# Optimization experiments

Measured on AMD Instinct MI355X. Metric: run time of the kernel, lower is better.

The kernel has to match this reference:

```python
import jax, jax.numpy as jnp
import numpy as np

TOPK = 8  # n_activated_experts


def setup_inputs() -> dict:
    key = jax.random.key(0)
    k1, k2 = jax.random.split(key)
    tokens, dim, n_experts = 8192, 4096, 64
    x = jax.random.normal(k1, (tokens, dim), dtype=jnp.float32)
    weight = jax.random.normal(k2, (n_experts, dim), dtype=jnp.float32) * 0.02
    bias = jnp.zeros((n_experts,), dtype=jnp.float32)
    return {"x": x, "weight": weight, "bias": bias}


def reference(x, weight, bias):
    # scores: [tokens, n_experts]
    scores = jnp.einsum("td,ed->te", x, weight) + bias
    probs = jax.nn.softmax(scores, axis=-1)  # score_func == 'softmax'
    weights, indices = jax.lax.top_k(probs, TOPK)
    return probs, indices
```

## Files before the change

### kernel.cpp

```cpp
#include <hip/hip_runtime.h>
#include <math.h>

#define NTOK    8192
#define DIM     4096
#define NEXP    64
#define TOPK_N  8
#define TAU     2.0e-4f
#define KSPLIT  8
#define KSTEPS  ((DIM / KSPLIT) / 32)
#define TB      16

#define WS_WHI_OFF  0
#define WS_WLO_OFF  524288

typedef __attribute__((ext_vector_type(8))) short short8;
typedef __attribute__((ext_vector_type(4))) float f32x4;

__device__ __forceinline__ void cvt8(float4 a0, float4 a1, short8& hv, short8& lv) {
    float f[8] = {a0.x, a0.y, a0.z, a0.w, a1.x, a1.y, a1.z, a1.w};
    union { short8 v; unsigned u[4]; } H, L;
    #pragma unroll
    for (int i = 0; i < 4; ++i) {
        unsigned b0 = __float_as_uint(f[2*i]);
        unsigned b1 = __float_as_uint(f[2*i+1]);
        float r0 = f[2*i]   - __uint_as_float(b0 & 0xffff0000u);
        float r1 = f[2*i+1] - __uint_as_float(b1 & 0xffff0000u);
        H.u[i] = (b0 >> 16) | (b1 & 0xffff0000u);
        L.u[i] = (__float_as_uint(r0) >> 16) | (__float_as_uint(r1) & 0xffff0000u);
    }
    hv = H.v; lv = L.v;
}

__global__ __launch_bounds__(256, 4)
void cvt_w_kernel(const float* __restrict__ w, unsigned short* __restrict__ whi,
                  unsigned short* __restrict__ wlo) {
    const int g = blockIdx.x * 256 + threadIdx.x;
    const float* p = w + (size_t)g * 8;
    union { short8 v; uint4 q; } H, L;
    float4 a0 = *(const float4*)(p);
    float4 a1 = *(const float4*)(p + 4);
    cvt8(a0, a1, H.v, L.v);
    *(uint4*)(whi + (size_t)g * 8) = H.q;
    *(uint4*)(wlo + (size_t)g * 8) = L.q;
}

__global__ __launch_bounds__(512, 4)
void gemm_kernel(const float* __restrict__ x, const unsigned short* __restrict__ whi,
                 const unsigned short* __restrict__ wlo, const float* __restrict__ bias,
                 const float* __restrict__ wfp, float* __restrict__ out, int ntok) {
    __shared__ float  lds_part[KSPLIT][TB][65];
    __shared__ float  lds_s[TB][68];
    __shared__ float  top9[TB][9];
    __shared__ double dsc[NEXP];
    __shared__ int    nflag;
    __shared__ int    ftok[TB];
    __shared__ float  fninth[TB];

    const int tid  = threadIdx.x;
    const int lane = tid & 63;
    const int wv   = tid >> 6;
    const int nl   = lane & 15;
    const int q    = lane >> 4;
    const int tok0 = blockIdx.x * TB;
    if (tid == 0) nflag = 0;

    const int kbase = wv * (DIM / KSPLIT);
    const float* xr = x + (size_t)(tok0 + nl) * DIM;
    size_t boff[4];
    #pragma unroll
    for (int nf = 0; nf < 4; ++nf) boff[nf] = (size_t)(nf * 16 + nl) * DIM;

    f32x4 acc[4];
    #pragma unroll
    for (int nf = 0; nf < 4; ++nf) acc[nf] = (f32x4){0.f, 0.f, 0.f, 0.f};

    float4 Ar[2][2];
    short8 Bh[2][4], Bl[2][4];

    {
        const int k0 = kbase + q * 8;
        Ar[0][0] = *(const float4*)(xr + k0);
        Ar[0][1] = *(const float4*)(xr + k0 + 4);
        #pragma unroll
        for (int nf = 0; nf < 4; ++nf) {
            Bh[0][nf] = *(const short8*)(whi + boff[nf] + k0);
            Bl[0][nf] = *(const short8*)(wlo + boff[nf] + k0);
        }
    }

    #pragma unroll 2
    for (int ks = 0; ks < KSTEPS; ++ks) {
        const int buf = ks & 1, nxt = buf ^ 1;
        if (ks + 1 < KSTEPS) {
            const int k1 = kbase + (ks + 1) * 32 + q * 8;
            Ar[nxt][0] = *(const float4*)(xr + k1);
            Ar[nxt][1] = *(const float4*)(xr + k1 + 4);
            #pragma unroll
            for (int nf = 0; nf < 4; ++nf) {
                Bh[nxt][nf] = *(const short8*)(whi + boff[nf] + k1);
                Bl[nxt][nf] = *(const short8*)(wlo + boff[nf] + k1);
            }
        }
        short8 ahi, alo;
        cvt8(Ar[buf][0], Ar[buf][1], ahi, alo);
        #pragma unroll
        for (int nf = 0; nf < 4; ++nf) {
            acc[nf] = __builtin_amdgcn_mfma_f32_16x16x32_bf16(ahi, Bl[buf][nf], acc[nf], 0, 0, 0);
            acc[nf] = __builtin_amdgcn_mfma_f32_16x16x32_bf16(alo, Bh[buf][nf], acc[nf], 0, 0, 0);
            acc[nf] = __builtin_amdgcn_mfma_f32_16x16x32_bf16(ahi, Bh[buf][nf], acc[nf], 0, 0, 0);
        }
    }

    #pragma unroll
    for (int nf = 0; nf < 4; ++nf)
        #pragma unroll
        for (int r = 0; r < 4; ++r)
            lds_part[wv][q * 4 + r][nf * 16 + nl] = acc[nf][r];
    __syncthreads();

    #pragma unroll
    for (int i = 0; i < (TB * NEXP) / 512; ++i) {
        const int p  = tid + i * 512;
        const int tk = p >> 6, e = p & 63;
        float s = lds_part[0][tk][e];
        #pragma unroll
        for (int k = 1; k < KSPLIT; ++k) s += lds_part[k][tk][e];
        lds_s[tk][e] = s + bias[e];
    }
    __syncthreads();

    float* __restrict__ out_idx = out + (size_t)ntok * NEXP;
    #pragma unroll
    for (int t = 0; t < 2; ++t) {
        const int tokl = wv * 2 + t;
        const int tok  = tok0 + tokl;
        const float s  = lds_s[tokl][lane];

        float m = s;
        #pragma unroll
        for (int off = 32; off > 0; off >>= 1)
            m = fmaxf(m, __shfl_xor(m, off, 64));
        const float ex = expf(s - m);
        float sum = ex;
        #pragma unroll
        for (int off = 32; off > 0; off >>= 1)
            sum += __shfl_xor(sum, off, 64);
        out[(size_t)tok * NEXP + lane] = ex / sum;

        int rank = 0;
        #pragma unroll
        for (int i = 0; i < 16; ++i) {
            const float4 v4 = *(const float4*)(&lds_s[tokl][i * 4]);
            rank += (int)((v4.x > s) || (v4.x == s && (i * 4 + 0) < lane));
            rank += (int)((v4.y > s) || (v4.y == s && (i * 4 + 1) < lane));
            rank += (int)((v4.z > s) || (v4.z == s && (i * 4 + 2) < lane));
            rank += (int)((v4.w > s) || (v4.w == s && (i * 4 + 3) < lane));
        }
        if (rank < TOPK_N + 1) top9[tokl][rank] = s;
        if (rank < TOPK_N)
            out_idx[(size_t)tok * TOPK_N + rank] = (float)lane;
    }
    __syncthreads();

    if (tid < TB) {
        float ming = 1e30f;
        #pragma unroll
        for (int r = 0; r < TOPK_N; ++r)
            ming = fminf(ming, top9[tid][r] - top9[tid][r + 1]);
        if (ming < TAU) {
            const int sl = atomicAdd(&nflag, 1);
            ftok[sl] = tid;
            fninth[sl] = top9[tid][TOPK_N];
        }
    }
    __syncthreads();

    const int nfl = nflag;
    for (int i = 0; i < nfl; ++i) {
        const int tokl = ftok[i];
        const int tok  = tok0 + tokl;
        const float thr = fninth[i] - TAU;
        const unsigned long long cmask = __ballot(lds_s[tokl][lane] >= thr);
        if (wv == 0) dsc[lane] = -1.0e300;
        __syncthreads();
        {
            int rank = 0;
            unsigned long long mm = cmask;
            while (mm) {
                const int e = __builtin_ctzll(mm);
                mm &= mm - 1;
                if ((rank & 7) == wv) {
                    const float* wr  = wfp + (size_t)e * DIM;
                    const float* xrr = x + (size_t)tok * DIM;
                    double a = 0.0;
                    #pragma unroll 4
                    for (int kk = 0; kk < 16; ++kk) {
                        const int k = kk * 256 + lane * 4;
                        const float4 wv4 = *(const float4*)(wr + k);
                        const float4 xv  = *(const float4*)(xrr + k);
                        a = fma((double)xv.x, (double)wv4.x, a);
                        a = fma((double)xv.y, (double)wv4.y, a);
                        a = fma((double)xv.z, (double)wv4.z, a);
                        a = fma((double)xv.w, (double)wv4.w, a);
                    }
                    #pragma unroll
                    for (int off = 32; off > 0; off >>= 1)
                        a += __shfl_xor(a, off, 64);
                    if (lane == 0) dsc[e] = a + (double)bias[e];
                }
                ++rank;
            }
        }
        __syncthreads();
        if (wv == 0) {
            double cv = dsc[lane];
            for (int r = 0; r < TOPK_N; ++r) {
                double bv = cv;
                int    bi = lane;
                #pragma unroll
                for (int off = 32; off > 0; off >>= 1) {
                    const double ov = __shfl_xor(bv, off, 64);
                    const int    oi = __shfl_xor(bi, off, 64);
                    if (ov > bv || (ov == bv && oi < bi)) { bv = ov; bi = oi; }
                }
                if (lane == r)
                    out_idx[(size_t)tok * TOPK_N + r] = (float)bi;
                if (lane == bi) cv = -1.0e301;
            }
        }
        __syncthreads();
    }
}

extern "C" void kernel_launch(void* const* d_in, const int* in_sizes, int n_in,
                              void* d_out, int out_size, void* d_ws, size_t ws_size,
                              hipStream_t stream) {
    const float* x  = (const float*)d_in[0];
    const float* w  = (const float*)d_in[1];
    const float* bs = (const float*)d_in[2];
    float* out = (float*)d_out;

    unsigned short* whi = (unsigned short*)((char*)d_ws + WS_WHI_OFF);
    unsigned short* wlo = (unsigned short*)((char*)d_ws + WS_WLO_OFF);

    const int ntok = in_sizes[0] / DIM;

    hipLaunchKernelGGL(cvt_w_kernel, dim3((NEXP * DIM) / 8 / 256), dim3(256), 0, stream,
                       w, whi, wlo);
    hipLaunchKernelGGL(gemm_kernel, dim3(ntok / TB), dim3(512), 0, stream,
                       x, whi, wlo, bs, w, out, ntok);
}
```

Baseline: 264.6 us.

## Double token tile per block to reuse weight fragments across two M groups

Each block now handles 32 tokens instead of 16, so every wave loads two 16-row x fragments and reuses the same bf16 hi/lo weight fragments across both, halving weight traffic per token. The k-loop is manually double-buffered with scheduling barriers between prefetch and compute phases. Launch bounds drop to 2 blocks per CU to allow for the larger register and LDS footprint, which lowers occupancy. The grid also halves to 256 blocks, which may leave some compute units with less latency hiding.

New measurement: 243.1 us. 8.1% less time.

```diff
diff --git a/kernel.cpp b/kernel.cpp
--- a/kernel.cpp
+++ b/kernel.cpp
@@ -8,7 +8,7 @@
 #define TAU     2.0e-4f
 #define KSPLIT  8
 #define KSTEPS  ((DIM / KSPLIT) / 32)
-#define TB      16
+#define TB      32
 
 #define WS_WHI_OFF  0
 #define WS_WLO_OFF  524288
@@ -44,7 +44,7 @@
     *(uint4*)(wlo + (size_t)g * 8) = L.q;
 }
 
-__global__ __launch_bounds__(512, 4)
+__global__ __launch_bounds__(512, 2)
 void gemm_kernel(const float* __restrict__ x, const unsigned short* __restrict__ whi,
                  const unsigned short* __restrict__ wlo, const float* __restrict__ bias,
                  const float* __restrict__ wfp, float* __restrict__ out, int ntok) {
@@ -65,57 +65,81 @@
     if (tid == 0) nflag = 0;
 
     const int kbase = wv * (DIM / KSPLIT);
-    const float* xr = x + (size_t)(tok0 + nl) * DIM;
+    const float* xr[2] = { x + (size_t)(tok0 + nl) * DIM,
+                           x + (size_t)(tok0 + 16 + nl) * DIM };
     size_t boff[4];
     #pragma unroll
     for (int nf = 0; nf < 4; ++nf) boff[nf] = (size_t)(nf * 16 + nl) * DIM;
 
-    f32x4 acc[4];
-    #pragma unroll
-    for (int nf = 0; nf < 4; ++nf) acc[nf] = (f32x4){0.f, 0.f, 0.f, 0.f};
-
-    float4 Ar[2][2];
+    f32x4 acc[2][4];
+    #pragma unroll
+    for (int mg = 0; mg < 2; ++mg)
+        #pragma unroll
+        for (int nf = 0; nf < 4; ++nf) acc[mg][nf] = (f32x4){0.f, 0.f, 0.f, 0.f};
+
+    float4 Ar[2][2][2];
     short8 Bh[2][4], Bl[2][4];
 
-    {
-        const int k0 = kbase + q * 8;
-        Ar[0][0] = *(const float4*)(xr + k0);
-        Ar[0][1] = *(const float4*)(xr + k0 + 4);
-        #pragma unroll
-        for (int nf = 0; nf < 4; ++nf) {
-            Bh[0][nf] = *(const short8*)(whi + boff[nf] + k0);
-            Bl[0][nf] = *(const short8*)(wlo + boff[nf] + k0);
-        }
-    }
-
-    #pragma unroll 2
-    for (int ks = 0; ks < KSTEPS; ++ks) {
-        const int buf = ks & 1, nxt = buf ^ 1;
-        if (ks + 1 < KSTEPS) {
-            const int k1 = kbase + (ks + 1) * 32 + q * 8;
-            Ar[nxt][0] = *(const float4*)(xr + k1);
-            Ar[nxt][1] = *(const float4*)(xr + k1 + 4);
+#define PREFETCH(nxt, ksx) do {                                            \
+        const int k1_ = kbase + (ksx) * 32 + q * 8;                        \
+        Ar[nxt][0][0] = *(const float4*)(xr[0] + k1_);                     \
+        Ar[nxt][0][1] = *(const float4*)(xr[0] + k1_ + 4);                 \
+        Ar[nxt][1][0] = *(const float4*)(xr[1] + k1_);                     \
+        Ar[nxt][1][1] = *(const float4*)(xr[1] + k1_ + 4);                 \
+        _Pragma("unroll")                                                  \
+        for (int nf_ = 0; nf_ < 4; ++nf_) {                                \
+            Bh[nxt][nf_] = *(const short8*)(whi + boff[nf_] + k1_);        \
+            Bl[nxt][nf_] = *(const short8*)(wlo + boff[nf_] + k1_);        \
+        }                                                                  \
+    } while (0)
+
+#define COMPUTE(buf) do {                                                  \
+        short8 ahi0_, alo0_, ahi1_, alo1_;                                 \
+        cvt8(Ar[buf][0][0], Ar[buf][0][1], ahi0_, alo0_);                  \
+        cvt8(Ar[buf][1][0], Ar[buf][1][1], ahi1_, alo1_);                  \
+        _Pragma("unroll")                                                  \
+        for (int nf_ = 0; nf_ < 4; ++nf_) {                                \
+            acc[0][nf_] = __builtin_amdgcn_mfma_f32_16x16x32_bf16(ahi0_, Bl[buf][nf_], acc[0][nf_], 0, 0, 0); \
+            acc[0][nf_] = __builtin_amdgcn_mfma_f32_16x16x32_bf16(alo0_, Bh[buf][nf_], acc[0][nf_], 0, 0, 0); \
+            acc[0][nf_] = __builtin_amdgcn_mfma_f32_16x16x32_bf16(ahi0_, Bh[buf][nf_], acc[0][nf_], 0, 0, 0); \
+            acc[1][nf_] = __builtin_amdgcn_mfma_f32_16x16x32_bf16(ahi1_, Bl[buf][nf_], acc[1][nf_], 0, 0, 0); \
+            acc[1][nf_] = __builtin_amdgcn_mfma_f32_16x16x32_bf16(alo1_, Bh[buf][nf_], acc[1][nf_], 0, 0, 0); \
+            acc[1][nf_] = __builtin_amdgcn_mfma_f32_16x16x32_bf16(ahi1_, Bh[buf][nf_], acc[1][nf_], 0, 0, 0); \
+        }                                                                  \
+    } while (0)
+
+#define WALL __builtin_amdgcn_sched_barrier(0)
+
+    PREFETCH(0, 0);
+    WALL;
+    #pragma unroll 1
+    for (int ks = 0; ks < KSTEPS - 2; ks += 2) {
+        PREFETCH(1, ks + 1);
+        WALL;
+        COMPUTE(0);
+        WALL;
+        PREFETCH(0, ks + 2);
+        WALL;
+        COMPUTE(1);
+        WALL;
+    }
+    PREFETCH(1, KSTEPS - 1);
+    WALL;
+    COMPUTE(0);
+    WALL;
+    COMPUTE(1);
+
+#undef PREFETCH
+#undef COMPUTE
+#undef WALL
+
+    #pragma unroll
+    for (int mg = 0; mg < 2; ++mg)
+        #pragma unroll
+        for (int nf = 0; nf < 4; ++nf)
             #pragma unroll
-            for (int nf = 0; nf < 4; ++nf) {
-                Bh[nxt][nf] = *(const short8*)(whi + boff[nf] + k1);
-                Bl[nxt][nf] = *(const short8*)(wlo + boff[nf] + k1);
-            }
-        }
-        short8 ahi, alo;
-        cvt8(Ar[buf][0], Ar[buf][1], ahi, alo);
-        #pragma unroll
-        for (int nf = 0; nf < 4; ++nf) {
-            acc[nf] = __builtin_amdgcn_mfma_f32_16x16x32_bf16(ahi, Bl[buf][nf], acc[nf], 0, 0, 0);
-            acc[nf] = __builtin_amdgcn_mfma_f32_16x16x32_bf16(alo, Bh[buf][nf], acc[nf], 0, 0, 0);
-            acc[nf] = __builtin_amdgcn_mfma_f32_16x16x32_bf16(ahi, Bh[buf][nf], acc[nf], 0, 0, 0);
-        }
-    }
-
-    #pragma unroll
-    for (int nf = 0; nf < 4; ++nf)
-        #pragma unroll
-        for (int r = 0; r < 4; ++r)
-            lds_part[wv][q * 4 + r][nf * 16 + nl] = acc[nf][r];
+            for (int r = 0; r < 4; ++r)
+                lds_part[wv][mg * 16 + q * 4 + r][nf * 16 + nl] = acc[mg][nf][r];
     __syncthreads();
 
     #pragma unroll
@@ -131,8 +155,8 @@
 
     float* __restrict__ out_idx = out + (size_t)ntok * NEXP;
     #pragma unroll
-    for (int t = 0; t < 2; ++t) {
-        const int tokl = wv * 2 + t;
+    for (int t = 0; t < 4; ++t) {
+        const int tokl = wv * 4 + t;
         const int tok  = tok0 + tokl;
         const float s  = lds_s[tokl][lane];
 
```

## Stage x and weight tiles through LDS with async loads and 32-token blocks

Applied to the files above, without the earlier changes.

Replaces the per-wave split-K GEMM, where each wave loaded its A and B fragments straight from global memory, with a double-buffered LDS-staged tile loop. It uses global_load_lds async copies with XOR swizzling and doubles the token block to 32. Waves now split the work into 4 K-slices by 2 expert halves, so the weight tile is shared across more tokens and the cross-wave reduction is smaller. In exchange it uses more LDS, lowers the occupancy target to 2 blocks, and adds a barrier every K step.

Result: faster. 251.9 us (-4.8%).

```diff
diff --git a/kernel.cpp b/kernel.cpp
--- a/kernel.cpp
+++ b/kernel.cpp
@@ -1,14 +1,13 @@
 #include <hip/hip_runtime.h>
 #include <math.h>
 
-#define NTOK    8192
 #define DIM     4096
 #define NEXP    64
 #define TOPK_N  8
 #define TAU     2.0e-4f
-#define KSPLIT  8
-#define KSTEPS  ((DIM / KSPLIT) / 32)
-#define TB      16
+#define TB      32
+#define BK      128
+#define KT      (DIM / BK)
 
 #define WS_WHI_OFF  0
 #define WS_WLO_OFF  524288
@@ -29,6 +28,12 @@
         L.u[i] = (__float_as_uint(r0) >> 16) | (__float_as_uint(r1) & 0xffff0000u);
     }
     hv = H.v; lv = L.v;
+}
+
+__device__ __forceinline__ void async16(void* lds, const void* g) {
+    __builtin_amdgcn_global_load_lds(
+        (const __attribute__((address_space(1))) unsigned int*)g,
+        (__attribute__((address_space(3))) unsigned int*)lds, 16, 0, 0);
 }
 
 __global__ __launch_bounds__(256, 4)
@@ -44,17 +49,26 @@
     *(uint4*)(wlo + (size_t)g * 8) = L.q;
 }
 
-__global__ __launch_bounds__(512, 4)
+__global__ __launch_bounds__(512, 2)
 void gemm_kernel(const float* __restrict__ x, const unsigned short* __restrict__ whi,
                  const unsigned short* __restrict__ wlo, const float* __restrict__ bias,
                  const float* __restrict__ wfp, float* __restrict__ out, int ntok) {
-    __shared__ float  lds_part[KSPLIT][TB][65];
-    __shared__ float  lds_s[TB][68];
-    __shared__ float  top9[TB][9];
-    __shared__ double dsc[NEXP];
-    __shared__ int    nflag;
-    __shared__ int    ftok[TB];
-    __shared__ float  fninth[TB];
+    __shared__ struct {
+        union {
+            struct {
+                float          A[2][TB][BK];
+                unsigned short Bh[2][NEXP][BK];
+                unsigned short Bl[2][NEXP][BK];
+            } st;
+            float part[4][TB][65];
+        } u;
+        float  s[TB][68];
+        float  top9[TB][9];
+        double dsc[NEXP];
+        int    nflag;
+        int    ftok[TB];
+        float  fninth[TB];
+    } sm;
 
     const int tid  = threadIdx.x;
     const int lane = tid & 63;
@@ -62,79 +76,111 @@
     const int nl   = lane & 15;
     const int q    = lane >> 4;
     const int tok0 = blockIdx.x * TB;
-    if (tid == 0) nflag = 0;
-
-    const int kbase = wv * (DIM / KSPLIT);
-    const float* xr = x + (size_t)(tok0 + nl) * DIM;
-    size_t boff[4];
-    #pragma unroll
-    for (int nf = 0; nf < 4; ++nf) boff[nf] = (size_t)(nf * 16 + nl) * DIM;
-
-    f32x4 acc[4];
-    #pragma unroll
-    for (int nf = 0; nf < 4; ++nf) acc[nf] = (f32x4){0.f, 0.f, 0.f, 0.f};
-
-    float4 Ar[2][2];
-    short8 Bh[2][4], Bl[2][4];
-
-    {
-        const int k0 = kbase + q * 8;
-        Ar[0][0] = *(const float4*)(xr + k0);
-        Ar[0][1] = *(const float4*)(xr + k0 + 4);
-        #pragma unroll
-        for (int nf = 0; nf < 4; ++nf) {
-            Bh[0][nf] = *(const short8*)(whi + boff[nf] + k0);
-            Bl[0][nf] = *(const short8*)(wlo + boff[nf] + k0);
-        }
-    }
-
+    if (tid == 0) sm.nflag = 0;
+
+    const int ss = wv & 3;
+    const int hf = wv >> 2;
+    const int abyte = ss * 128 + q * 32;
+    const int bbyte = ss * 64 + q * 16;
+
+    int arow0[2], be0[2];
+    const float* gA[2];
+    const unsigned short *gBh[2], *gBl[2];
+    #pragma unroll
+    for (int i = 0; i < 2; ++i) {
+        arow0[i] = wv * 4 + i * 2;
+        const int ra = arow0[i] + (lane >> 5);
+        gA[i] = x + (size_t)(tok0 + ra) * DIM + (((lane & 31) * 4) ^ ((ra & 7) << 2));
+        be0[i] = wv * 8 + i * 4;
+        const int ea = be0[i] + (lane >> 4);
+        const int el = (((lane & 15) * 8) ^ ((ea & 7) << 3));
+        gBh[i] = whi + (size_t)ea * DIM + el;
+        gBl[i] = wlo + (size_t)ea * DIM + el;
+    }
+
+    f32x4 acc[2][2];
+    #pragma unroll
+    for (int mg = 0; mg < 2; ++mg)
+        #pragma unroll
+        for (int nf = 0; nf < 2; ++nf) acc[mg][nf] = (f32x4){0.f, 0.f, 0.f, 0.f};
+
+#define STAGE(b_, k0_) do {                                                    \
+        _Pragma("unroll")                                                      \
+        for (int i_ = 0; i_ < 2; ++i_) {                                       \
+            async16(&sm.u.st.A[b_][arow0[i_]][0],  gA[i_]  + (k0_));           \
+            async16(&sm.u.st.Bh[b_][be0[i_]][0],   gBh[i_] + (k0_));           \
+            async16(&sm.u.st.Bl[b_][be0[i_]][0],   gBl[i_] + (k0_));           \
+        }                                                                      \
+    } while (0)
+
+#define COMPUTE(b_) do {                                                       \
+        short8 ahi_[2], alo_[2], bh_[2], bl_[2];                               \
+        _Pragma("unroll")                                                      \
+        for (int mg_ = 0; mg_ < 2; ++mg_) {                                    \
+            const int r_ = mg_ * 16 + nl;                                      \
+            const char* rp_ = (const char*)&sm.u.st.A[b_][r_][0];              \
+            const int sw_ = (r_ & 7) << 4;                                     \
+            float4 a0_ = *(const float4*)(rp_ + (abyte ^ sw_));                \
+            float4 a1_ = *(const float4*)(rp_ + ((abyte + 16) ^ sw_));         \
+            cvt8(a0_, a1_, ahi_[mg_], alo_[mg_]);                              \
+        }                                                                      \
+        _Pragma("unroll")                                                      \
+        for (int nf_ = 0; nf_ < 2; ++nf_) {                                    \
+            const int e_ = (hf * 2 + nf_) * 16 + nl;                           \
+            const int sw_ = (e_ & 7) << 4;                                     \
+            bh_[nf_] = *(const short8*)((const char*)&sm.u.st.Bh[b_][e_][0] + (bbyte ^ sw_)); \
+            bl_[nf_] = *(const short8*)((const char*)&sm.u.st.Bl[b_][e_][0] + (bbyte ^ sw_)); \
+        }                                                                      \
+        _Pragma("unroll")                                                      \
+        for (int mg_ = 0; mg_ < 2; ++mg_)                                      \
+            _Pragma("unroll")                                                  \
+            for (int nf_ = 0; nf_ < 2; ++nf_) {                                \
+                acc[mg_][nf_] = __builtin_amdgcn_mfma_f32_16x16x32_bf16(ahi_[mg_], bl_[nf_], acc[mg_][nf_], 0, 0, 0); \
+                acc[mg_][nf_] = __builtin_amdgcn_mfma_f32_16x16x32_bf16(alo_[mg_], bh_[nf_], acc[mg_][nf_], 0, 0, 0); \
+                acc[mg_][nf_] = __builtin_amdgcn_mfma_f32_16x16x32_bf16(ahi_[mg_], bh_[nf_], acc[mg_][nf_], 0, 0, 0); \
+            }                                                                  \
+    } while (0)
+
+    STAGE(0, 0);
+    __syncthreads();
     #pragma unroll 2
-    for (int ks = 0; ks < KSTEPS; ++ks) {
-        const int buf = ks & 1, nxt = buf ^ 1;
-        if (ks + 1 < KSTEPS) {
-            const int k1 = kbase + (ks + 1) * 32 + q * 8;
-            Ar[nxt][0] = *(const float4*)(xr + k1);
-            Ar[nxt][1] = *(const float4*)(xr + k1 + 4);
+    for (int kt = 0; kt < KT; ++kt) {
+        const int b = kt & 1;
+        if (kt + 1 < KT) STAGE(b ^ 1, (kt + 1) * BK);
+        __builtin_amdgcn_sched_barrier(0);
+        COMPUTE(b);
+        __syncthreads();
+    }
+
+#undef STAGE
+#undef COMPUTE
+
+    #pragma unroll
+    for (int mg = 0; mg < 2; ++mg)
+        #pragma unroll
+        for (int nf = 0; nf < 2; ++nf)
             #pragma unroll
-            for (int nf = 0; nf < 4; ++nf) {
-                Bh[nxt][nf] = *(const short8*)(whi + boff[nf] + k1);
-                Bl[nxt][nf] = *(const short8*)(wlo + boff[nf] + k1);
-            }
-        }
-        short8 ahi, alo;
-        cvt8(Ar[buf][0], Ar[buf][1], ahi, alo);
-        #pragma unroll
-        for (int nf = 0; nf < 4; ++nf) {
-            acc[nf] = __builtin_amdgcn_mfma_f32_16x16x32_bf16(ahi, Bl[buf][nf], acc[nf], 0, 0, 0);
-            acc[nf] = __builtin_amdgcn_mfma_f32_16x16x32_bf16(alo, Bh[buf][nf], acc[nf], 0, 0, 0);
-            acc[nf] = __builtin_amdgcn_mfma_f32_16x16x32_bf16(ahi, Bh[buf][nf], acc[nf], 0, 0, 0);
-        }
-    }
-
-    #pragma unroll
-    for (int nf = 0; nf < 4; ++nf)
-        #pragma unroll
-        for (int r = 0; r < 4; ++r)
-            lds_part[wv][q * 4 + r][nf * 16 + nl] = acc[nf][r];
+            for (int r = 0; r < 4; ++r)
+                sm.u.part[ss][mg * 16 + q * 4 + r][(hf * 2 + nf) * 16 + nl] = acc[mg][nf][r];
     __syncthreads();
 
     #pragma unroll
     for (int i = 0; i < (TB * NEXP) / 512; ++i) {
         const int p  = tid + i * 512;
         const int tk = p >> 6, e = p & 63;
-        float s = lds_part[0][tk][e];
-        #pragma unroll
-        for (int k = 1; k < KSPLIT; ++k) s += lds_part[k][tk][e];
-        lds_s[tk][e] = s + bias[e];
+        float s = sm.u.part[0][tk][e];
+        #pragma unroll
+        for (int k = 1; k < 4; ++k) s += sm.u.part[k][tk][e];
+        sm.s[tk][e] = s + bias[e];
     }
     __syncthreads();
 
     float* __restrict__ out_idx = out + (size_t)ntok * NEXP;
     #pragma unroll
-    for (int t = 0; t < 2; ++t) {
-        const int tokl = wv * 2 + t;
+    for (int t = 0; t < 4; ++t) {
+        const int tokl = wv * 4 + t;
         const int tok  = tok0 + tokl;
-        const float s  = lds_s[tokl][lane];
+        const float s  = sm.s[tokl][lane];
 
         float m = s;
         #pragma unroll
@@ -150,13 +196,13 @@
         int rank = 0;
         #pragma unroll
         for (int i = 0; i < 16; ++i) {
-            const float4 v4 = *(const float4*)(&lds_s[tokl][i * 4]);
+            const float4 v4 = *(const float4*)(&sm.s[tokl][i * 4]);
             rank += (int)((v4.x > s) || (v4.x == s && (i * 4 + 0) < lane));
             rank += (int)((v4.y > s) || (v4.y == s && (i * 4 + 1) < lane));
             rank += (int)((v4.z > s) || (v4.z == s && (i * 4 + 2) < lane));
             rank += (int)((v4.w > s) || (v4.w == s && (i * 4 + 3) < lane));
         }
-        if (rank < TOPK_N + 1) top9[tokl][rank] = s;
+        if (rank < TOPK_N + 1) sm.top9[tokl][rank] = s;
         if (rank < TOPK_N)
             out_idx[(size_t)tok * TOPK_N + rank] = (float)lane;
     }
@@ -166,22 +212,22 @@
         float ming = 1e30f;
         #pragma unroll
         for (int r = 0; r < TOPK_N; ++r)
-            ming = fminf(ming, top9[tid][r] - top9[tid][r + 1]);
+            ming = fminf(ming, sm.top9[tid][r] - sm.top9[tid][r + 1]);
         if (ming < TAU) {
-            const int sl = atomicAdd(&nflag, 1);
-            ftok[sl] = tid;
-            fninth[sl] = top9[tid][TOPK_N];
-        }
-    }
-    __syncthreads();
-
-    const int nfl = nflag;
+            const int sl = atomicAdd(&sm.nflag, 1);
+            sm.ftok[sl] = tid;
+            sm.fninth[sl] = sm.top9[tid][TOPK_N];
+        }
+    }
+    __syncthreads();
+
+    const int nfl = sm.nflag;
     for (int i = 0; i < nfl; ++i) {
-        const int tokl = ftok[i];
+        const int tokl = sm.ftok[i];
         const int tok  = tok0 + tokl;
-        const float thr = fninth[i] - TAU;
-        const unsigned long long cmask = __ballot(lds_s[tokl][lane] >= thr);
-        if (wv == 0) dsc[lane] = -1.0e300;
+        const float thr = sm.fninth[i] - TAU;
+        const unsigned long long cmask = __ballot(sm.s[tokl][lane] >= thr);
+        if (wv == 0) sm.dsc[lane] = -1.0e300;
         __syncthreads();
         {
             int rank = 0;
@@ -206,14 +252,14 @@
                     #pragma unroll
                     for (int off = 32; off > 0; off >>= 1)
                         a += __shfl_xor(a, off, 64);
-                    if (lane == 0) dsc[e] = a + (double)bias[e];
+                    if (lane == 0) sm.dsc[e] = a + (double)bias[e];
                 }
                 ++rank;
             }
         }
         __syncthreads();
         if (wv == 0) {
-            double cv = dsc[lane];
+            double cv = sm.dsc[lane];
             for (int r = 0; r < TOPK_N; ++r) {
                 double bv = cv;
                 int    bi = lane;
```

## Split GEMM over K-chunk blocks with partial buffer and separate finish kernel

Applied to the files above, without the earlier changes.

Replaces the single fused kernel with a split-K GEMM kernel, where each block covers 64 tokens by 512 K. Partial sums go to a workspace buffer, or are atomically added into the output if the workspace is too small. A separate finish kernel then does the reduction, softmax, top-k and the fp64 tie-break recheck per wavefront. Weight fragments are now loaded inside the loop instead of being double-buffered, and sched barriers pin instruction order. The goal is to raise parallelism and drop the block-level syncs, at the cost of extra global traffic for the partials and one more launch.

Result: no change. 263.0 us (-0.6%).

```diff
diff --git a/kernel.cpp b/kernel.cpp
--- a/kernel.cpp
+++ b/kernel.cpp
@@ -1,20 +1,23 @@
 #include <hip/hip_runtime.h>
 #include <math.h>
 
-#define NTOK    8192
 #define DIM     4096
 #define NEXP    64
 #define TOPK_N  8
 #define TAU     2.0e-4f
-#define KSPLIT  8
-#define KSTEPS  ((DIM / KSPLIT) / 32)
-#define TB      16
+#define TGB     64
+#define KC      512
+#define NKC     (DIM / KC)
+#define KS32    (KC / 32)
 
 #define WS_WHI_OFF  0
-#define WS_WLO_OFF  524288
+#define WS_WLO_OFF  (512*1024)
+#define WS_PART_OFF (1024*1024)
 
 typedef __attribute__((ext_vector_type(8))) short short8;
 typedef __attribute__((ext_vector_type(4))) float f32x4;
+
+#define WALL __builtin_amdgcn_sched_barrier(0)
 
 __device__ __forceinline__ void cvt8(float4 a0, float4 a1, short8& hv, short8& lv) {
     float f[8] = {a0.x, a0.y, a0.z, a0.w, a1.x, a1.y, a1.z, a1.w};
@@ -44,191 +47,178 @@
     *(uint4*)(wlo + (size_t)g * 8) = L.q;
 }
 
-__global__ __launch_bounds__(512, 4)
-void gemm_kernel(const float* __restrict__ x, const unsigned short* __restrict__ whi,
-                 const unsigned short* __restrict__ wlo, const float* __restrict__ bias,
-                 const float* __restrict__ wfp, float* __restrict__ out, int ntok) {
-    __shared__ float  lds_part[KSPLIT][TB][65];
-    __shared__ float  lds_s[TB][68];
-    __shared__ float  top9[TB][9];
-    __shared__ double dsc[NEXP];
-    __shared__ int    nflag;
-    __shared__ int    ftok[TB];
-    __shared__ float  fninth[TB];
+__global__ __launch_bounds__(256, 4)
+void zero_kernel(float* __restrict__ p) {
+    const size_t g = (size_t)blockIdx.x * 256 + threadIdx.x;
+    *(float4*)(p + g * 4) = (float4){0.f, 0.f, 0.f, 0.f};
+}
+
+template<int USE_PART>
+__global__ __launch_bounds__(256, 4)
+void gemm_part_kernel(const float* __restrict__ x, const unsigned short* __restrict__ whi,
+                      const unsigned short* __restrict__ wlo, float* __restrict__ dst,
+                      int ntok) {
+    const int tid  = threadIdx.x;
+    const int lane = tid & 63;
+    const int wvm  = tid >> 6;
+    const int nl   = lane & 15;
+    const int q    = lane >> 4;
+    const int kc   = blockIdx.x & (NKC - 1);
+    const int tg   = blockIdx.x >> 3;
+    const int t0   = tg * TGB + wvm * 16;
+    const int k0   = kc * KC;
+
+    const float* xr = x + (size_t)(t0 + nl) * DIM + k0;
+    const unsigned short* bh[4];
+    const unsigned short* bl[4];
+    #pragma unroll
+    for (int nf = 0; nf < 4; ++nf) {
+        const size_t o = (size_t)(nf * 16 + nl) * DIM + k0;
+        bh[nf] = whi + o;
+        bl[nf] = wlo + o;
+    }
+
+    f32x4 acc[4];
+    #pragma unroll
+    for (int nf = 0; nf < 4; ++nf) acc[nf] = (f32x4){0.f, 0.f, 0.f, 0.f};
+
+    float4 Ar[2][2];
+    Ar[0][0] = *(const float4*)(xr + q * 8);
+    Ar[0][1] = *(const float4*)(xr + q * 8 + 4);
+
+    #pragma unroll 2
+    for (int s = 0; s < KS32; ++s) {
+        const int buf = s & 1;
+        if (s + 1 < KS32) {
+            const int kk = (s + 1) * 32 + q * 8;
+            Ar[buf ^ 1][0] = *(const float4*)(xr + kk);
+            Ar[buf ^ 1][1] = *(const float4*)(xr + kk + 4);
+        }
+        WALL;
+        const int kk = s * 32 + q * 8;
+        short8 bhv[4], blv[4];
+        #pragma unroll
+        for (int nf = 0; nf < 4; ++nf) {
+            bhv[nf] = *(const short8*)(bh[nf] + kk);
+            blv[nf] = *(const short8*)(bl[nf] + kk);
+        }
+        short8 ahi, alo;
+        cvt8(Ar[buf][0], Ar[buf][1], ahi, alo);
+        #pragma unroll
+        for (int nf = 0; nf < 4; ++nf) {
+            acc[nf] = __builtin_amdgcn_mfma_f32_16x16x32_bf16(ahi, blv[nf], acc[nf], 0, 0, 0);
+            acc[nf] = __builtin_amdgcn_mfma_f32_16x16x32_bf16(alo, bhv[nf], acc[nf], 0, 0, 0);
+            acc[nf] = __builtin_amdgcn_mfma_f32_16x16x32_bf16(ahi, bhv[nf], acc[nf], 0, 0, 0);
+        }
+        WALL;
+    }
+
+    #pragma unroll
+    for (int nf = 0; nf < 4; ++nf)
+        #pragma unroll
+        for (int r = 0; r < 4; ++r) {
+            const int tok = t0 + q * 4 + r;
+            const int e   = nf * 16 + nl;
+            if (USE_PART)
+                dst[((size_t)tok * NKC + kc) * NEXP + e] = acc[nf][r];
+            else
+                atomicAdd(&dst[(size_t)tok * NEXP + e], acc[nf][r]);
+        }
+}
+
+template<int USE_PART>
+__global__ __launch_bounds__(256, 4)
+void finish_kernel(const float* __restrict__ src, const float* __restrict__ bias,
+                   const float* __restrict__ x, const float* __restrict__ wfp,
+                   float* __restrict__ out, int ntok) {
+    __shared__ float lds_s[4][68];
+    __shared__ float t9[4][12];
 
     const int tid  = threadIdx.x;
     const int lane = tid & 63;
     const int wv   = tid >> 6;
-    const int nl   = lane & 15;
-    const int q    = lane >> 4;
-    const int tok0 = blockIdx.x * TB;
-    if (tid == 0) nflag = 0;
-
-    const int kbase = wv * (DIM / KSPLIT);
-    const float* xr = x + (size_t)(tok0 + nl) * DIM;
-    size_t boff[4];
-    #pragma unroll
-    for (int nf = 0; nf < 4; ++nf) boff[nf] = (size_t)(nf * 16 + nl) * DIM;
-
-    f32x4 acc[4];
-    #pragma unroll
-    for (int nf = 0; nf < 4; ++nf) acc[nf] = (f32x4){0.f, 0.f, 0.f, 0.f};
-
-    float4 Ar[2][2];
-    short8 Bh[2][4], Bl[2][4];
-
-    {
-        const int k0 = kbase + q * 8;
-        Ar[0][0] = *(const float4*)(xr + k0);
-        Ar[0][1] = *(const float4*)(xr + k0 + 4);
-        #pragma unroll
-        for (int nf = 0; nf < 4; ++nf) {
-            Bh[0][nf] = *(const short8*)(whi + boff[nf] + k0);
-            Bl[0][nf] = *(const short8*)(wlo + boff[nf] + k0);
-        }
-    }
-
-    #pragma unroll 2
-    for (int ks = 0; ks < KSTEPS; ++ks) {
-        const int buf = ks & 1, nxt = buf ^ 1;
-        if (ks + 1 < KSTEPS) {
-            const int k1 = kbase + (ks + 1) * 32 + q * 8;
-            Ar[nxt][0] = *(const float4*)(xr + k1);
-            Ar[nxt][1] = *(const float4*)(xr + k1 + 4);
+    const int tok  = blockIdx.x * 4 + wv;
+
+    float s;
+    if (USE_PART) {
+        const float* pr = src + (size_t)tok * NKC * NEXP;
+        s = pr[lane];
+        #pragma unroll
+        for (int c = 1; c < NKC; ++c) s += pr[c * NEXP + lane];
+    } else {
+        s = src[(size_t)tok * NEXP + lane];
+    }
+    s += bias[lane];
+
+    float m = s;
+    #pragma unroll
+    for (int off = 32; off > 0; off >>= 1)
+        m = fmaxf(m, __shfl_xor(m, off, 64));
+    const float ex = expf(s - m);
+    float sum = ex;
+    #pragma unroll
+    for (int off = 32; off > 0; off >>= 1)
+        sum += __shfl_xor(sum, off, 64);
+    out[(size_t)tok * NEXP + lane] = ex / sum;
+
+    lds_s[wv][lane] = s;
+    int rank = 0;
+    #pragma unroll
+    for (int i = 0; i < 16; ++i) {
+        const float4 v4 = *(const float4*)(&lds_s[wv][i * 4]);
+        rank += (int)((v4.x > s) || (v4.x == s && (i * 4 + 0) < lane));
+        rank += (int)((v4.y > s) || (v4.y == s && (i * 4 + 1) < lane));
+        rank += (int)((v4.z > s) || (v4.z == s && (i * 4 + 2) < lane));
+        rank += (int)((v4.w > s) || (v4.w == s && (i * 4 + 3) < lane));
+    }
+    float* __restrict__ out_idx = out + (size_t)ntok * NEXP;
+    if (rank < TOPK_N + 1) t9[wv][rank] = s;
+    if (rank < TOPK_N)
+        out_idx[(size_t)tok * TOPK_N + rank] = (float)lane;
+
+    float gap = 1e30f;
+    if (lane < TOPK_N) gap = t9[wv][lane] - t9[wv][lane + 1];
+    if (__any(gap < TAU)) {
+        const float thr = t9[wv][TOPK_N] - TAU;
+        const unsigned long long cmask = __ballot(s >= thr);
+        double dscv = -1.0e300;
+        unsigned long long mm = cmask;
+        while (mm) {
+            const int e = __builtin_ctzll(mm);
+            mm &= mm - 1;
+            const float* wr  = wfp + (size_t)e * DIM;
+            const float* xrr = x + (size_t)tok * DIM;
+            double a = 0.0;
+            #pragma unroll 4
+            for (int kk = 0; kk < 16; ++kk) {
+                const int k = kk * 256 + lane * 4;
+                const float4 wv4 = *(const float4*)(wr + k);
+                const float4 xv  = *(const float4*)(xrr + k);
+                a = fma((double)xv.x, (double)wv4.x, a);
+                a = fma((double)xv.y, (double)wv4.y, a);
+                a = fma((double)xv.z, (double)wv4.z, a);
+                a = fma((double)xv.w, (double)wv4.w, a);
+            }
             #pragma unroll
-            for (int nf = 0; nf < 4; ++nf) {
-                Bh[nxt][nf] = *(const short8*)(whi + boff[nf] + k1);
-                Bl[nxt][nf] = *(const short8*)(wlo + boff[nf] + k1);
+            for (int off = 32; off > 0; off >>= 1)
+                a += __shfl_xor(a, off, 64);
+            a += (double)bias[e];
+            if (lane == e) dscv = a;
+        }
+        double cv = dscv;
+        for (int r = 0; r < TOPK_N; ++r) {
+            double bv = cv;
+            int    bi = lane;
+            #pragma unroll
+            for (int off = 32; off > 0; off >>= 1) {
+                const double ov = __shfl_xor(bv, off, 64);
+                const int    oi = __shfl_xor(bi, off, 64);
+                if (ov > bv || (ov == bv && oi < bi)) { bv = ov; bi = oi; }
             }
-        }
-        short8 ahi, alo;
-        cvt8(Ar[buf][0], Ar[buf][1], ahi, alo);
-        #pragma unroll
-        for (int nf = 0; nf < 4; ++nf) {
-            acc[nf] = __builtin_amdgcn_mfma_f32_16x16x32_bf16(ahi, Bl[buf][nf], acc[nf], 0, 0, 0);
-            acc[nf] = __builtin_amdgcn_mfma_f32_16x16x32_bf16(alo, Bh[buf][nf], acc[nf], 0, 0, 0);
-            acc[nf] = __builtin_amdgcn_mfma_f32_16x16x32_bf16(ahi, Bh[buf][nf], acc[nf], 0, 0, 0);
-        }
-    }
-
-    #pragma unroll
-    for (int nf = 0; nf < 4; ++nf)
-        #pragma unroll
-        for (int r = 0; r < 4; ++r)
-            lds_part[wv][q * 4 + r][nf * 16 + nl] = acc[nf][r];
-    __syncthreads();
-
-    #pragma unroll
-    for (int i = 0; i < (TB * NEXP) / 512; ++i) {
-        const int p  = tid + i * 512;
-        const int tk = p >> 6, e = p & 63;
-        float s = lds_part[0][tk][e];
-        #pragma unroll
-        for (int k = 1; k < KSPLIT; ++k) s += lds_part[k][tk][e];
-        lds_s[tk][e] = s + bias[e];
-    }
-    __syncthreads();
-
-    float* __restrict__ out_idx = out + (size_t)ntok * NEXP;
-    #pragma unroll
-    for (int t = 0; t < 2; ++t) {
-        const int tokl = wv * 2 + t;
-        const int tok  = tok0 + tokl;
-        const float s  = lds_s[tokl][lane];
-
-        float m = s;
-        #pragma unroll
-        for (int off = 32; off > 0; off >>= 1)
-            m = fmaxf(m, __shfl_xor(m, off, 64));
-        const float ex = expf(s - m);
-        float sum = ex;
-        #pragma unroll
-        for (int off = 32; off > 0; off >>= 1)
-            sum += __shfl_xor(sum, off, 64);
-        out[(size_t)tok * NEXP + lane] = ex / sum;
-
-        int rank = 0;
-        #pragma unroll
-        for (int i = 0; i < 16; ++i) {
-            const float4 v4 = *(const float4*)(&lds_s[tokl][i * 4]);
-            rank += (int)((v4.x > s) || (v4.x == s && (i * 4 + 0) < lane));
-            rank += (int)((v4.y > s) || (v4.y == s && (i * 4 + 1) < lane));
-            rank += (int)((v4.z > s) || (v4.z == s && (i * 4 + 2) < lane));
-            rank += (int)((v4.w > s) || (v4.w == s && (i * 4 + 3) < lane));
-        }
-        if (rank < TOPK_N + 1) top9[tokl][rank] = s;
-        if (rank < TOPK_N)
-            out_idx[(size_t)tok * TOPK_N + rank] = (float)lane;
-    }
-    __syncthreads();
-
-    if (tid < TB) {
-        float ming = 1e30f;
-        #pragma unroll
-        for (int r = 0; r < TOPK_N; ++r)
-            ming = fminf(ming, top9[tid][r] - top9[tid][r + 1]);
-        if (ming < TAU) {
-            const int sl = atomicAdd(&nflag, 1);
-            ftok[sl] = tid;
-            fninth[sl] = top9[tid][TOPK_N];
-        }
-    }
-    __syncthreads();
-
-    const int nfl = nflag;
-    for (int i = 0; i < nfl; ++i) {
-        const int tokl = ftok[i];
-        const int tok  = tok0 + tokl;
-        const float thr = fninth[i] - TAU;
-        const unsigned long long cmask = __ballot(lds_s[tokl][lane] >= thr);
-        if (wv == 0) dsc[lane] = -1.0e300;
-        __syncthreads();
-        {
-            int rank = 0;
-            unsigned long long mm = cmask;
-            while (mm) {
-                const int e = __builtin_ctzll(mm);
-                mm &= mm - 1;
-                if ((rank & 7) == wv) {
-                    const float* wr  = wfp + (size_t)e * DIM;
-                    const float* xrr = x + (size_t)tok * DIM;
-                    double a = 0.0;
-                    #pragma unroll 4
-                    for (int kk = 0; kk < 16; ++kk) {
-                        const int k = kk * 256 + lane * 4;
-                        const float4 wv4 = *(const float4*)(wr + k);
-                        const float4 xv  = *(const float4*)(xrr + k);
-                        a = fma((double)xv.x, (double)wv4.x, a);
-                        a = fma((double)xv.y, (double)wv4.y, a);
-                        a = fma((double)xv.z, (double)wv4.z, a);
-                        a = fma((double)xv.w, (double)wv4.w, a);
-                    }
-                    #pragma unroll
-                    for (int off = 32; off > 0; off >>= 1)
-                        a += __shfl_xor(a, off, 64);
-                    if (lane == 0) dsc[e] = a + (double)bias[e];
-                }
-                ++rank;
-            }
-        }
-        __syncthreads();
-        if (wv == 0) {
-            double cv = dsc[lane];
-            for (int r = 0; r < TOPK_N; ++r) {
-                double bv = cv;
-                int    bi = lane;
-                #pragma unroll
-                for (int off = 32; off > 0; off >>= 1) {
-                    const double ov = __shfl_xor(bv, off, 64);
-                    const int    oi = __shfl_xor(bi, off, 64);
-                    if (ov > bv || (ov == bv && oi < bi)) { bv = ov; bi = oi; }
-                }
-                if (lane == r)
-                    out_idx[(size_t)tok * TOPK_N + r] = (float)bi;
-                if (lane == bi) cv = -1.0e301;
-            }
-        }
-        __syncthreads();
+            if (lane == r)
+                out_idx[(size_t)tok * TOPK_N + r] = (float)bi;
+            if (lane == bi) cv = -1.0e301;
+        }
     }
 }
 
@@ -247,6 +237,19 @@
 
     hipLaunchKernelGGL(cvt_w_kernel, dim3((NEXP * DIM) / 8 / 256), dim3(256), 0, stream,
                        w, whi, wlo);
-    hipLaunchKernelGGL(gemm_kernel, dim3(ntok / TB), dim3(512), 0, stream,
-                       x, whi, wlo, bs, w, out, ntok);
-}
+
+    const size_t part_need = (size_t)WS_PART_OFF + (size_t)ntok * NKC * NEXP * sizeof(float);
+    if (ws_size >= part_need) {
+        float* part = (float*)((char*)d_ws + WS_PART_OFF);
+        hipLaunchKernelGGL((gemm_part_kernel<1>), dim3((ntok / TGB) * NKC), dim3(256), 0, stream,
+                           x, whi, wlo, part, ntok);
+        hipLaunchKernelGGL((finish_kernel<1>), dim3(ntok / 4), dim3(256), 0, stream,
+                           part, bs, x, w, out, ntok);
+    } else {
+        hipLaunchKernelGGL(zero_kernel, dim3((ntok * NEXP) / 1024), dim3(256), 0, stream, out);
+        hipLaunchKernelGGL((gemm_part_kernel<0>), dim3((ntok / TGB) * NKC), dim3(256), 0, stream,
+                           x, whi, wlo, out, ntok);
+        hipLaunchKernelGGL((finish_kernel<0>), dim3(ntok / 4), dim3(256), 0, stream,
+                           out, bs, x, w, out, ntok);
+    }
+}
```
